# Optimization experiments

Hardware: AMD Instinct MI355X
Metric: run time of the kernel (lower is better)

## Reference

```python
import jax, jax.numpy as jnp
import numpy as np

NEG_SLOPE = 0.01  # torch nn.LeakyReLU default


def setup_inputs() -> dict:
    key = jax.random.key(0)
    k1, k2, k3 = jax.random.split(key, 3)
    B, H, D, L = 4, 8, 64, 2048
    q = jax.random.normal(k1, (B, H, D, L), dtype=jnp.float32)
    k = jax.random.normal(k2, (B, H, D, L), dtype=jnp.float32)
    v = jax.random.normal(k3, (B, H, D, L), dtype=jnp.float32)
    return {"q": q, "k": k, "v": v}


def reference(q, k, v):
    # q, k, v: [B, H, D, L] (note: feature dim BEFORE length, as in the torch module)
    d_tensor = q.shape[2]
    scale = 1.0 / np.sqrt(d_tensor).astype(np.float32)
    # scores = LeakyReLU(q^T k / sqrt(d)) : [B, H, Lq, Lk]
    scores = jnp.einsum('bhdq,bhdk->bhqk', q, k) * scale
    scores = jax.nn.leaky_relu(scores, negative_slope=NEG_SLOPE)
    psi = jax.nn.softmax(scores, axis=-1)
    # out = (psi @ v^T)^T : [B, H, D, Lq]
    out = jnp.einsum('bhqk,bhdk->bhdq', psi, v)
    return out
```

## Files before the change

kernel.cpp:

```cpp
#include <hip/hip_runtime.h>
#include <math.h>

#define DD 64
#define LL 2048
#define NHEADS 32
#define NTHREADS 512
#define TQ 64
#define TK 128
#define NTILES (LL / TK)
#define FTQ 128
#define FTK 64
#define FNTILES (LL / FTK)
#define QSCALE 0.18033688011112042f

typedef __bf16 bf16_t;
typedef __bf16 bf16x8 __attribute__((ext_vector_type(8)));
typedef float f32x16 __attribute__((ext_vector_type(16)));

struct __align__(16) SMemM {
  bf16_t Qs[TQ][72];
  bf16_t Ks[TK][72];
  bf16_t Vs[DD][136];
};
struct __align__(16) SMemME {
  float Oe1[TQ][65];
  float Oe2[TQ][65];
};
union __align__(16) SMemMU { SMemM a; SMemME e; };

struct __align__(16) SMemF {
  bf16_t Qs[FTQ][72];
  bf16_t Ks[FTK][72];
  bf16_t Vs[DD][72];
};
union __align__(16) SMemFU { SMemF a; float Oe[FTQ][65]; };

__global__ __launch_bounds__(256)
void prep(const float* __restrict__ k, const float* __restrict__ v,
          bf16_t* __restrict__ Kt, bf16_t* __restrict__ Vb) {
  const int bid = blockIdx.x;
  const int tid = threadIdx.x;
  if (bid < 1024) {
    const int head = bid >> 5;
    const int l0   = (bid & 31) * 64;
    const float* sp = k + (size_t)head * DD * LL;
    bf16_t* dp = Kt + ((size_t)head * LL + l0) * DD;
    const int lk = tid & 63;
    const int dg = (tid >> 6) * 8;
    for (int rep = 0; rep < 2; ++rep) {
      const int d0 = dg + rep * 32;
      bf16x8 pk;
      for (int j = 0; j < 8; ++j)
        pk[j] = (bf16_t)sp[(size_t)(d0 + j) * LL + l0 + lk];
      *(bf16x8*)(dp + (size_t)lk * DD + d0) = pk;
    }
  } else {
    size_t i = ((size_t)(bid - 1024) * 256 + tid) * 8;
    float4 a = *(const float4*)(v + i);
    float4 b = *(const float4*)(v + i + 4);
    bf16x8 p;
    p[0] = (bf16_t)a.x; p[1] = (bf16_t)a.y; p[2] = (bf16_t)a.z; p[3] = (bf16_t)a.w;
    p[4] = (bf16_t)b.x; p[5] = (bf16_t)b.y; p[6] = (bf16_t)b.z; p[7] = (bf16_t)b.w;
    *(bf16x8*)(Vb + i) = p;
  }
}

__global__ __launch_bounds__(NTHREADS, 4)
void attn_main(const float* __restrict__ q, const bf16_t* __restrict__ Kt,
               const bf16_t* __restrict__ Vb, float* __restrict__ out) {
  __shared__ SMemMU sm;
  __shared__ float rsA[TQ], rsB[TQ];
  const int tid  = threadIdx.x;
  const int w    = tid >> 6;
  const int lane = tid & 63;
  const int l31  = lane & 31;
  const int hh   = lane >> 5;
  const int strip = w & 1;
  const int quart = w >> 1;
  const int wbase = strip * 32;
  const int lkh   = quart * 32;
  const int head = blockIdx.y;
  const int q0   = blockIdx.x * TQ;
  const float*  qp = q  + (size_t)head * DD * LL;
  const bf16_t* kp = Kt + (size_t)head * LL * DD;
  const bf16_t* vp = Vb + (size_t)head * DD * LL;

  {
    const int lq = tid & 63;
    const int d0 = (tid >> 6) * 8;
    const float* src = qp + q0 + lq;
    bf16x8 pk;
    for (int j = 0; j < 8; ++j)
      pk[j] = (bf16_t)(src[(size_t)(d0 + j) * LL] * QSCALE);
    *(bf16x8*)&sm.a.Qs[lq][d0] = pk;
  }

  const int klk  = tid & 127;
  const int kd0  = (tid >> 7) * 16;
  const int vd   = tid >> 3;
  const int vc16 = (tid & 7) * 16;

  bf16x8 kr0 = *(const bf16x8*)(kp + (size_t)klk * DD + kd0);
  bf16x8 kr1 = *(const bf16x8*)(kp + (size_t)klk * DD + kd0 + 8);
  bf16x8 vr0 = *(const bf16x8*)(vp + (size_t)vd * LL + vc16);
  bf16x8 vr1 = *(const bf16x8*)(vp + (size_t)vd * LL + vc16 + 8);

  __syncthreads();
  bf16x8 bq[4];
  for (int kk = 0; kk < 4; ++kk)
    bq[kk] = *(const bf16x8*)&sm.a.Qs[wbase + l31][kk * 16 + 8 * hh];

  f32x16 oacc[2];
  for (int dt = 0; dt < 2; ++dt)
    for (int r = 0; r < 16; ++r) oacc[dt][r] = 0.f;
  float rsum = 0.f;

  for (int t = 0; t < NTILES; ++t) {
    __syncthreads();
    *(bf16x8*)&sm.a.Ks[klk][kd0]      = kr0;
    *(bf16x8*)&sm.a.Ks[klk][kd0 + 8]  = kr1;
    *(bf16x8*)&sm.a.Vs[vd][vc16]      = vr0;
    *(bf16x8*)&sm.a.Vs[vd][vc16 + 8]  = vr1;
    __syncthreads();

    if (t + 1 < NTILES) {
      const int lk0n = (t + 1) * TK;
      kr0 = *(const bf16x8*)(kp + (size_t)(lk0n + klk) * DD + kd0);
      kr1 = *(const bf16x8*)(kp + (size_t)(lk0n + klk) * DD + kd0 + 8);
      vr0 = *(const bf16x8*)(vp + (size_t)vd * LL + lk0n + vc16);
      vr1 = *(const bf16x8*)(vp + (size_t)vd * LL + lk0n + vc16 + 8);
    }

    f32x16 st;
    for (int r = 0; r < 16; ++r) st[r] = 0.f;
    for (int kk = 0; kk < 4; ++kk) {
      bf16x8 ak = *(const bf16x8*)&sm.a.Ks[lkh + l31][kk * 16 + 8 * hh];
      st = __builtin_amdgcn_mfma_f32_32x32x16_bf16(ak, bq[kk], st, 0, 0, 0);
    }

    unsigned pb[8];
    for (int r = 0; r < 16; ++r) {
      float s = st[r];
      s = fmaxf(s, 0.01f * s);
      float p = __builtin_amdgcn_exp2f(s);
      rsum += p;
      st[r] = p;
    }
    for (int qq = 0; qq < 8; ++qq) {
      union { bf16_t b[2]; unsigned u; } pk;
      pk.b[0] = (bf16_t)st[2 * qq];
      pk.b[1] = (bf16_t)st[2 * qq + 1];
      pb[qq] = pk.u;
    }

    for (int kk2 = 0; kk2 < 2; ++kk2) {
      unsigned l0 = pb[4 * kk2 + 0], l1 = pb[4 * kk2 + 1];
      unsigned l2 = pb[4 * kk2 + 2], l3 = pb[4 * kk2 + 3];
      unsigned s0 = hh ? l0 : l2;
      unsigned s1 = hh ? l1 : l3;
      unsigned f0 = (unsigned)__shfl_xor((int)s0, 32);
      unsigned f1 = (unsigned)__shfl_xor((int)s1, 32);
      union { unsigned u[4]; bf16x8 v; } ap;
      ap.u[0] = hh ? f0 : l0;
      ap.u[1] = hh ? f1 : l1;
      ap.u[2] = hh ? l2 : f0;
      ap.u[3] = hh ? l3 : f1;
      const int lkb = lkh + kk2 * 16 + 8 * hh;
      for (int dt = 0; dt < 2; ++dt) {
        bf16x8 bv = *(const bf16x8*)&sm.a.Vs[dt * 32 + l31][lkb];
        oacc[dt] = __builtin_amdgcn_mfma_f32_32x32x16_bf16(ap.v, bv, oacc[dt], 0, 0, 0);
      }
    }
  }

  float rtot = rsum + __shfl_xor(rsum, 32);
  __syncthreads();
  if (quart == 0) {
    rsA[wbase + l31] = rtot;
    for (int r = 0; r < 16; ++r) {
      int row = (r & 3) + 8 * (r >> 2) + 4 * hh;
      for (int dt = 0; dt < 2; ++dt)
        sm.e.Oe1[wbase + row][dt * 32 + l31] = oacc[dt][r];
    }
  } else if (quart == 2) {
    rsB[wbase + l31] = rtot;
    for (int r = 0; r < 16; ++r) {
      int row = (r & 3) + 8 * (r >> 2) + 4 * hh;
      for (int dt = 0; dt < 2; ++dt)
        sm.e.Oe2[wbase + row][dt * 32 + l31] = oacc[dt][r];
    }
  }
  __syncthreads();
  if (quart == 1) {
    rsA[wbase + l31] += rtot;
    for (int r = 0; r < 16; ++r) {
      int row = (r & 3) + 8 * (r >> 2) + 4 * hh;
      for (int dt = 0; dt < 2; ++dt)
        sm.e.Oe1[wbase + row][dt * 32 + l31] += oacc[dt][r];
    }
  } else if (quart == 3) {
    rsB[wbase + l31] += rtot;
    for (int r = 0; r < 16; ++r) {
      int row = (r & 3) + 8 * (r >> 2) + 4 * hh;
      for (int dt = 0; dt < 2; ++dt)
        sm.e.Oe2[wbase + row][dt * 32 + l31] += oacc[dt][r];
    }
  }
  __syncthreads();
  if (tid < TQ) rsA[tid] = 1.0f / (rsA[tid] + rsB[tid]);
  __syncthreads();
  float* op = out + (size_t)head * DD * LL + q0;
  for (int i = 0; i < 8; ++i) {
    int idx = tid + NTHREADS * i;
    int d   = idx >> 6;
    int lq  = idx & 63;
    op[(size_t)d * LL + lq] = (sm.e.Oe1[lq][d] + sm.e.Oe2[lq][d]) * rsA[lq];
  }
}

__global__ __launch_bounds__(NTHREADS, 4)
void attn_flash_fb(const float* __restrict__ q, const float* __restrict__ k,
                   const float* __restrict__ v, float* __restrict__ out) {
  __shared__ SMemFU sm;
  __shared__ float rs1[FTQ];
  const int tid  = threadIdx.x;
  const int w    = tid >> 6;
  const int lane = tid & 63;
  const int l31  = lane & 31;
  const int hh   = lane >> 5;
  const int strip = w & 3;
  const int half  = w >> 2;
  const int wbase = strip * 32;
  const int lkh   = half * 32;
  const int head = blockIdx.y;
  const int q0   = blockIdx.x * FTQ;
  const size_t hoff = (size_t)head * DD * LL;
  const float* qp = q + hoff;
  const float* kp = k + hoff;
  const float* vp = v + hoff;
  {
    int lq  = tid & 127;
    int d0q = (tid >> 7) * 16;
    const float* src = qp + q0 + lq;
    for (int g = 0; g < 2; ++g) {
      bf16x8 pk;
      for (int j = 0; j < 8; ++j)
        pk[j] = (bf16_t)(src[(size_t)(d0q + g * 8 + j) * LL] * QSCALE);
      *(bf16x8*)&sm.a.Qs[lq][d0q + g * 8] = pk;
    }
  }
  const int klk = tid & 63;
  const int kd0 = (tid >> 6) * 8;
  const int vd  = tid >> 3;
  const int vc8 = (tid & 7) * 8;
  float  kreg[8];
  float4 vreg[2];
  {
    const float* ks = kp + klk;
    for (int j = 0; j < 8; ++j) kreg[j] = ks[(size_t)(kd0 + j) * LL];
    vreg[0] = *(const float4*)(vp + (size_t)vd * LL + vc8);
    vreg[1] = *(const float4*)(vp + (size_t)vd * LL + vc8 + 4);
  }
  __syncthreads();
  bf16x8 bq[4];
  for (int kk = 0; kk < 4; ++kk)
    bq[kk] = *(const bf16x8*)&sm.a.Qs[wbase + l31][kk * 16 + 8 * hh];
  f32x16 oacc[2];
  for (int dt = 0; dt < 2; ++dt)
    for (int r = 0; r < 16; ++r) oacc[dt][r] = 0.f;
  float rsum = 0.f;
  for (int t = 0; t < FNTILES; ++t) {
    __syncthreads();
    {
      bf16x8 pk;
      for (int j = 0; j < 8; ++j) pk[j] = (bf16_t)kreg[j];
      *(bf16x8*)&sm.a.Ks[klk][kd0] = pk;
      bf16x8 pv;
      pv[0] = (bf16_t)vreg[0].x; pv[1] = (bf16_t)vreg[0].y;
      pv[2] = (bf16_t)vreg[0].z; pv[3] = (bf16_t)vreg[0].w;
      pv[4] = (bf16_t)vreg[1].x; pv[5] = (bf16_t)vreg[1].y;
      pv[6] = (bf16_t)vreg[1].z; pv[7] = (bf16_t)vreg[1].w;
      *(bf16x8*)&sm.a.Vs[vd][vc8] = pv;
    }
    __syncthreads();
    if (t + 1 < FNTILES) {
      const int lk0n = (t + 1) * FTK;
      const float* ks = kp + lk0n + klk;
      for (int j = 0; j < 8; ++j) kreg[j] = ks[(size_t)(kd0 + j) * LL];
      vreg[0] = *(const float4*)(vp + (size_t)vd * LL + lk0n + vc8);
      vreg[1] = *(const float4*)(vp + (size_t)vd * LL + lk0n + vc8 + 4);
    }
    f32x16 st;
    for (int r = 0; r < 16; ++r) st[r] = 0.f;
    for (int kk = 0; kk < 4; ++kk) {
      bf16x8 ak = *(const bf16x8*)&sm.a.Ks[lkh + l31][kk * 16 + 8 * hh];
      st = __builtin_amdgcn_mfma_f32_32x32x16_bf16(ak, bq[kk], st, 0, 0, 0);
    }
    unsigned pb[8];
    for (int r = 0; r < 16; ++r) {
      float s = st[r];
      s = fmaxf(s, 0.01f * s);
      float p = __builtin_amdgcn_exp2f(s);
      rsum += p;
      st[r] = p;
    }
    for (int qq = 0; qq < 8; ++qq) {
      union { bf16_t b[2]; unsigned u; } pk;
      pk.b[0] = (bf16_t)st[2 * qq];
      pk.b[1] = (bf16_t)st[2 * qq + 1];
      pb[qq] = pk.u;
    }
    for (int kk2 = 0; kk2 < 2; ++kk2) {
      unsigned l0 = pb[4 * kk2 + 0], l1 = pb[4 * kk2 + 1];
      unsigned l2 = pb[4 * kk2 + 2], l3 = pb[4 * kk2 + 3];
      unsigned s0 = hh ? l0 : l2;
      unsigned s1 = hh ? l1 : l3;
      unsigned f0 = (unsigned)__shfl_xor((int)s0, 32);
      unsigned f1 = (unsigned)__shfl_xor((int)s1, 32);
      union { unsigned u[4]; bf16x8 v; } ap;
      ap.u[0] = hh ? f0 : l0;
      ap.u[1] = hh ? f1 : l1;
      ap.u[2] = hh ? l2 : f0;
      ap.u[3] = hh ? l3 : f1;
      const int lkb = lkh + kk2 * 16 + 8 * hh;
      for (int dt = 0; dt < 2; ++dt) {
        bf16x8 bv = *(const bf16x8*)&sm.a.Vs[dt * 32 + l31][lkb];
        oacc[dt] = __builtin_amdgcn_mfma_f32_32x32x16_bf16(ap.v, bv, oacc[dt], 0, 0, 0);
      }
    }
  }
  float rtot = rsum + __shfl_xor(rsum, 32);
  __syncthreads();
  if (half == 1) {
    rs1[wbase + l31] = rtot;
    for (int r = 0; r < 16; ++r) {
      int row = (r & 3) + 8 * (r >> 2) + 4 * hh;
      for (int dt = 0; dt < 2; ++dt)
        sm.Oe[wbase + row][dt * 32 + l31] = oacc[dt][r];
    }
  }
  __syncthreads();
  if (half == 0) {
    float tot = rtot + rs1[wbase + l31];
    rs1[wbase + l31] = 1.0f / tot;
    float inv[16];
    for (int r = 0; r < 16; ++r) {
      int row = (r & 3) + 8 * (r >> 2) + 4 * hh;
      inv[r] = rs1[wbase + row];
    }
    for (int r = 0; r < 16; ++r) {
      int row = (r & 3) + 8 * (r >> 2) + 4 * hh;
      for (int dt = 0; dt < 2; ++dt) {
        int col = dt * 32 + l31;
        sm.Oe[wbase + row][col] = (oacc[dt][r] + sm.Oe[wbase + row][col]) * inv[r];
      }
    }
  }
  __syncthreads();
  float* op = out + hoff + q0;
  for (int i = 0; i < 16; ++i) {
    int idx = tid + NTHREADS * i;
    int d   = idx >> 7;
    int lq  = idx & 127;
    op[(size_t)d * LL + lq] = sm.Oe[lq][d];
  }
}

extern "C" void kernel_launch(void* const* d_in, const int* in_sizes, int n_in,
                              void* d_out, int out_size, void* d_ws, size_t ws_size,
                              hipStream_t stream) {
  const float* q = (const float*)d_in[0];
  const float* k = (const float*)d_in[1];
  const float* v = (const float*)d_in[2];
  float* out = (float*)d_out;
  const size_t tsz  = (size_t)NHEADS * LL * DD;
  const size_t need = 2 * tsz * sizeof(bf16_t);
  if (ws_size >= need) {
    bf16_t* Kt = (bf16_t*)d_ws;
    bf16_t* Vb = Kt + tsz;
    prep<<<1024 + 2048, 256, 0, stream>>>(k, v, Kt, Vb);
    dim3 grid(LL / TQ, NHEADS);
    attn_main<<<grid, NTHREADS, 0, stream>>>(q, Kt, Vb, out);
  } else {
    dim3 grid(LL / FTQ, NHEADS);
    attn_flash_fb<<<grid, NTHREADS, 0, stream>>>(q, k, v, out);
  }
}
```

Before: 155.4 us.

## Double-buffer K/V tiles in LDS and retile main attention kernel to TQ=128

The main attention kernel now works on 128 query rows per block with 64-key tiles. K/V tiles are double-buffered in LDS, so each tile needs one barrier instead of two, and the next tile's global loads overlap with compute. Waves are split into 4 query strips by 2 key halves, which shrinks the cross-wave reduction epilogue to a single partial-sum exchange with the normalization fused in. Each K/V tile is now reused across twice as many queries, but the grid has half as many blocks, which may hurt occupancy and load balance across CUs.

```diff
diff --git a/kernel.cpp b/kernel.cpp
--- a/kernel.cpp
+++ b/kernel.cpp
@@ -5,8 +5,8 @@
 #define LL 2048
 #define NHEADS 32
 #define NTHREADS 512
-#define TQ 64
-#define TK 128
+#define TQ 128
+#define TK 64
 #define NTILES (LL / TK)
 #define FTQ 128
 #define FTK 64
@@ -19,14 +19,13 @@
 
 struct __align__(16) SMemM {
   bf16_t Qs[TQ][72];
-  bf16_t Ks[TK][72];
-  bf16_t Vs[DD][136];
+  bf16_t Ks[2][TK][72];
+  bf16_t Vs[2][DD][72];
 };
-struct __align__(16) SMemME {
-  float Oe1[TQ][65];
-  float Oe2[TQ][65];
+union __align__(16) SMemMU {
+  SMemM a;
+  float Oe[TQ][65];
 };
-union __align__(16) SMemMU { SMemM a; SMemME e; };
 
 struct __align__(16) SMemF {
   bf16_t Qs[FTQ][72];
@@ -69,43 +68,44 @@
 void attn_main(const float* __restrict__ q, const bf16_t* __restrict__ Kt,
                const bf16_t* __restrict__ Vb, float* __restrict__ out) {
   __shared__ SMemMU sm;
-  __shared__ float rsA[TQ], rsB[TQ];
+  __shared__ float rs1[TQ];
   const int tid  = threadIdx.x;
   const int w    = tid >> 6;
   const int lane = tid & 63;
   const int l31  = lane & 31;
   const int hh   = lane >> 5;
-  const int strip = w & 1;
-  const int quart = w >> 1;
+  const int strip = w & 3;
+  const int half  = w >> 2;
   const int wbase = strip * 32;
-  const int lkh   = quart * 32;
+  const int lkh   = half * 32;
   const int head = blockIdx.y;
   const int q0   = blockIdx.x * TQ;
   const float*  qp = q  + (size_t)head * DD * LL;
   const bf16_t* kp = Kt + (size_t)head * LL * DD;
   const bf16_t* vp = Vb + (size_t)head * DD * LL;
 
+  const int klk = tid & 63;
+  const int kd0 = (tid >> 6) * 8;
+  const int vd  = tid >> 3;
+  const int vc8 = (tid & 7) * 8;
+
+  bf16x8 kr = *(const bf16x8*)(kp + (size_t)klk * DD + kd0);
+  bf16x8 vr = *(const bf16x8*)(vp + (size_t)vd * LL + vc8);
+
   {
-    const int lq = tid & 63;
-    const int d0 = (tid >> 6) * 8;
+    const int lq = tid & 127;
+    const int d0 = (tid >> 7) * 16;
     const float* src = qp + q0 + lq;
-    bf16x8 pk;
-    for (int j = 0; j < 8; ++j)
-      pk[j] = (bf16_t)(src[(size_t)(d0 + j) * LL] * QSCALE);
-    *(bf16x8*)&sm.a.Qs[lq][d0] = pk;
-  }
-
-  const int klk  = tid & 127;
-  const int kd0  = (tid >> 7) * 16;
-  const int vd   = tid >> 3;
-  const int vc16 = (tid & 7) * 16;
-
-  bf16x8 kr0 = *(const bf16x8*)(kp + (size_t)klk * DD + kd0);
-  bf16x8 kr1 = *(const bf16x8*)(kp + (size_t)klk * DD + kd0 + 8);
-  bf16x8 vr0 = *(const bf16x8*)(vp + (size_t)vd * LL + vc16);
-  bf16x8 vr1 = *(const bf16x8*)(vp + (size_t)vd * LL + vc16 + 8);
-
-  __syncthreads();
+    bf16x8 p0, p1;
+    for (int j = 0; j < 8; ++j) {
+      p0[j] = (bf16_t)(src[(size_t)(d0 + j) * LL] * QSCALE);
+      p1[j] = (bf16_t)(src[(size_t)(d0 + 8 + j) * LL] * QSCALE);
+    }
+    *(bf16x8*)&sm.a.Qs[lq][d0]     = p0;
+    *(bf16x8*)&sm.a.Qs[lq][d0 + 8] = p1;
+  }
+  __syncthreads();
+
   bf16x8 bq[4];
   for (int kk = 0; kk < 4; ++kk)
     bq[kk] = *(const bf16x8*)&sm.a.Qs[wbase + l31][kk * 16 + 8 * hh];
@@ -115,29 +115,19 @@
     for (int r = 0; r < 16; ++r) oacc[dt][r] = 0.f;
   float rsum = 0.f;
 
-  for (int t = 0; t < NTILES; ++t) {
-    __syncthreads();
-    *(bf16x8*)&sm.a.Ks[klk][kd0]      = kr0;
-    *(bf16x8*)&sm.a.Ks[klk][kd0 + 8]  = kr1;
-    *(bf16x8*)&sm.a.Vs[vd][vc16]      = vr0;
-    *(bf16x8*)&sm.a.Vs[vd][vc16 + 8]  = vr1;
-    __syncthreads();
-
-    if (t + 1 < NTILES) {
-      const int lk0n = (t + 1) * TK;
-      kr0 = *(const bf16x8*)(kp + (size_t)(lk0n + klk) * DD + kd0);
-      kr1 = *(const bf16x8*)(kp + (size_t)(lk0n + klk) * DD + kd0 + 8);
-      vr0 = *(const bf16x8*)(vp + (size_t)vd * LL + lk0n + vc16);
-      vr1 = *(const bf16x8*)(vp + (size_t)vd * LL + lk0n + vc16 + 8);
-    }
-
+  *(bf16x8*)&sm.a.Ks[0][klk][kd0] = kr;
+  *(bf16x8*)&sm.a.Vs[0][vd][vc8]  = vr;
+  kr = *(const bf16x8*)(kp + (size_t)(TK + klk) * DD + kd0);
+  vr = *(const bf16x8*)(vp + (size_t)vd * LL + TK + vc8);
+  __syncthreads();
+
+  auto compute_tile = [&](int buf) {
     f32x16 st;
     for (int r = 0; r < 16; ++r) st[r] = 0.f;
     for (int kk = 0; kk < 4; ++kk) {
-      bf16x8 ak = *(const bf16x8*)&sm.a.Ks[lkh + l31][kk * 16 + 8 * hh];
+      bf16x8 ak = *(const bf16x8*)&sm.a.Ks[buf][lkh + l31][kk * 16 + 8 * hh];
       st = __builtin_amdgcn_mfma_f32_32x32x16_bf16(ak, bq[kk], st, 0, 0, 0);
     }
-
     unsigned pb[8];
     for (int r = 0; r < 16; ++r) {
       float s = st[r];
@@ -152,7 +142,6 @@
       pk.b[1] = (bf16_t)st[2 * qq + 1];
       pb[qq] = pk.u;
     }
-
     for (int kk2 = 0; kk2 < 2; ++kk2) {
       unsigned l0 = pb[4 * kk2 + 0], l1 = pb[4 * kk2 + 1];
       unsigned l2 = pb[4 * kk2 + 2], l3 = pb[4 * kk2 + 3];
@@ -167,54 +156,67 @@
       ap.u[3] = hh ? l3 : f1;
       const int lkb = lkh + kk2 * 16 + 8 * hh;
       for (int dt = 0; dt < 2; ++dt) {
-        bf16x8 bv = *(const bf16x8*)&sm.a.Vs[dt * 32 + l31][lkb];
+        bf16x8 bv = *(const bf16x8*)&sm.a.Vs[buf][dt * 32 + l31][lkb];
         oacc[dt] = __builtin_amdgcn_mfma_f32_32x32x16_bf16(ap.v, bv, oacc[dt], 0, 0, 0);
       }
     }
+  };
+
+  for (int i = 0; i < NTILES / 2; ++i) {
+    *(bf16x8*)&sm.a.Ks[1][klk][kd0] = kr;
+    *(bf16x8*)&sm.a.Vs[1][vd][vc8]  = vr;
+    {
+      const int tn = (2 * i + 2 < NTILES) ? (2 * i + 2) : (NTILES - 1);
+      kr = *(const bf16x8*)(kp + (size_t)(tn * TK + klk) * DD + kd0);
+      vr = *(const bf16x8*)(vp + (size_t)vd * LL + tn * TK + vc8);
+    }
+    compute_tile(0);
+    __syncthreads();
+
+    *(bf16x8*)&sm.a.Ks[0][klk][kd0] = kr;
+    *(bf16x8*)&sm.a.Vs[0][vd][vc8]  = vr;
+    {
+      const int tn = (2 * i + 3 < NTILES) ? (2 * i + 3) : (NTILES - 1);
+      kr = *(const bf16x8*)(kp + (size_t)(tn * TK + klk) * DD + kd0);
+      vr = *(const bf16x8*)(vp + (size_t)vd * LL + tn * TK + vc8);
+    }
+    compute_tile(1);
+    __syncthreads();
   }
 
   float rtot = rsum + __shfl_xor(rsum, 32);
-  __syncthreads();
-  if (quart == 0) {
-    rsA[wbase + l31] = rtot;
+  if (half == 1) {
+    rs1[wbase + l31] = rtot;
     for (int r = 0; r < 16; ++r) {
       int row = (r & 3) + 8 * (r >> 2) + 4 * hh;
       for (int dt = 0; dt < 2; ++dt)
-        sm.e.Oe1[wbase + row][dt * 32 + l31] = oacc[dt][r];
-    }
-  } else if (quart == 2) {
-    rsB[wbase + l31] = rtot;
-    for (int r = 0; r < 16; ++r) {
-      int row = (r & 3) + 8 * (r >> 2) + 4 * hh;
-      for (int dt = 0; dt < 2; ++dt)
-        sm.e.Oe2[wbase + row][dt * 32 + l31] = oacc[dt][r];
-    }
-  }
-  __syncthreads();
-  if (quart == 1) {
-    rsA[wbase + l31] += rtot;
-    for (int r = 0; r < 16; ++r) {
-      int row = (r & 3) + 8 * (r >> 2) + 4 * hh;
-      for (int dt = 0; dt < 2; ++dt)
-        sm.e.Oe1[wbase + row][dt * 32 + l31] += oacc[dt][r];
-    }
-  } else if (quart == 3) {
-    rsB[wbase + l31] += rtot;
-    for (int r = 0; r < 16; ++r) {
-      int row = (r & 3) + 8 * (r >> 2) + 4 * hh;
-      for (int dt = 0; dt < 2; ++dt)
-        sm.e.Oe2[wbase + row][dt * 32 + l31] += oacc[dt][r];
-    }
-  }
-  __syncthreads();
-  if (tid < TQ) rsA[tid] = 1.0f / (rsA[tid] + rsB[tid]);
+        sm.Oe[wbase + row][dt * 32 + l31] = oacc[dt][r];
+    }
+  }
+  __syncthreads();
+  if (half == 0) {
+    float tot = rtot + rs1[wbase + l31];
+    rs1[wbase + l31] = 1.0f / tot;
+    float inv[16];
+    for (int r = 0; r < 16; ++r) {
+      int row = (r & 3) + 8 * (r >> 2) + 4 * hh;
+      inv[r] = rs1[wbase + row];
+    }
+    for (int r = 0; r < 16; ++r) {
+      int row = (r & 3) + 8 * (r >> 2) + 4 * hh;
+      for (int dt = 0; dt < 2; ++dt) {
+        int col = dt * 32 + l31;
+        sm.Oe[wbase + row][col] = (oacc[dt][r] + sm.Oe[wbase + row][col]) * inv[r];
+      }
+    }
+  }
   __syncthreads();
   float* op = out + (size_t)head * DD * LL + q0;
-  for (int i = 0; i < 8; ++i) {
+  for (int i = 0; i < 16; ++i) {
     int idx = tid + NTHREADS * i;
-    int d   = idx >> 6;
-    int lq  = idx & 63;
-    op[(size_t)d * LL + lq] = (sm.e.Oe1[lq][d] + sm.e.Oe2[lq][d]) * rsA[lq];
+    int d   = idx >> 7;
+    int lq  = idx & 127;
+    op[(size_t)d * LL + lq] = sm.Oe[lq][d];
   }
 }
 
```

Result: faster. 149.1 us (-4.1%).
